# Optimization experiments

Hardware: AMD Instinct MI355X
Metric: run time of the kernel (lower is better)

## Reference

```python
import jax, jax.numpy as jnp
import numpy as np

N = 10000
E = 320000
NDIM_IN = 128
EDIM = 128
NDIM_OUT = 128
HID = 152  # size_embedding
NCLS = 15  # nbclasses


def _lin(k, out_f, in_f, scale=0.05):
    kw, kb = jax.random.split(k)
    W = jax.random.normal(kw, (out_f, in_f), dtype=jnp.float32) * scale
    b = jax.random.normal(kb, (out_f,), dtype=jnp.float32) * scale
    return W, b


def setup_inputs() -> dict:
    key = jax.random.key(0)
    ks = jax.random.split(key, 12)
    nfeats = jax.random.normal(ks[0], (N, 1, NDIM_IN), dtype=jnp.float32)
    efeats = jax.random.normal(ks[1], (E, 1, EDIM), dtype=jnp.float32)
    src = jax.random.randint(ks[2], (E,), 0, N)
    dst = jax.random.randint(ks[3], (E,), 0, N)
    # SAGE layer 1: msg (ndim_in+edim -> 152), apply (ndim_in+152 -> 152)
    Wm1, bm1 = _lin(ks[4], HID, NDIM_IN + EDIM)
    Wa1, ba1 = _lin(ks[5], HID, NDIM_IN + HID)
    # layer 2: msg (152+edim -> 152), apply (152+152 -> 152)
    Wm2, bm2 = _lin(ks[6], HID, HID + EDIM)
    Wa2, ba2 = _lin(ks[7], HID, HID + HID)
    # layer 3: msg (152+edim -> ndim_out), apply (152+ndim_out -> ndim_out)
    Wm3, bm3 = _lin(ks[8], NDIM_OUT, HID + EDIM)
    Wa3, ba3 = _lin(ks[9], NDIM_OUT, HID + NDIM_OUT)
    # edge predictor: Linear(2*ndim_out -> nbclasses)
    Wp, bp = _lin(ks[10], NCLS, 2 * NDIM_OUT)
    return {"nfeats": nfeats, "efeats": efeats, "src": src, "dst": dst,
            "Wm1": Wm1, "bm1": bm1, "Wa1": Wa1, "ba1": ba1,
            "Wm2": Wm2, "bm2": bm2, "Wa2": Wa2, "ba2": ba2,
            "Wm3": Wm3, "bm3": bm3, "Wa3": Wa3, "ba3": ba3,
            "Wp": Wp, "bp": bp}


def _sage_layer(h, e, src, dst, Wm, bm, Wa, ba):
    # h: [N,1,din]  e: [E,1,edim]
    msg = jnp.concatenate([h[src], e], axis=-1) @ Wm.T + bm  # [E,1,dout]
    agg = jax.ops.segment_sum(msg, dst, num_segments=N)       # [N,1,dout]
    deg = jax.ops.segment_sum(jnp.ones((E,), dtype=h.dtype), dst, num_segments=N)
    h_neigh = agg / jnp.maximum(deg, 1.0)[:, None, None]      # mean; 0 for isolated nodes
    return jax.nn.relu(jnp.concatenate([h, h_neigh], axis=-1) @ Wa.T + ba)


def reference(nfeats, efeats, src, dst,
              Wm1, bm1, Wa1, ba1, Wm2, bm2, Wa2, ba2,
              Wm3, bm3, Wa3, ba3, Wp, bp):
    h = _sage_layer(nfeats, efeats, src, dst, Wm1, bm1, Wa1, ba1)
    h = _sage_layer(h, efeats, src, dst, Wm2, bm2, Wa2, ba2)  # dropout is identity in eval
    h = _sage_layer(h, efeats, src, dst, Wm3, bm3, Wa3, ba3)
    h = h.sum(axis=1)  # [N, ndim_out]
    v = jnp.concatenate([h[src], h[dst]], axis=1)  # [E, 2*ndim_out]
    return v @ Wp.T + bp  # [E, nbclasses]
```

## Files before the change

### kernel.cpp

```cpp
#include <hip/hip_runtime.h>
#include <hip/hip_bf16.h>
#include <cstdint>


static inline int cdiv(int a, int b) { return (a + b - 1) / b; }

#define NN 10000
#define NE 320000
#define MTB 313

typedef __attribute__((ext_vector_type(8))) short bf16x8;
typedef __attribute__((ext_vector_type(4))) float f32x4;

__device__ __forceinline__ ushort f2bf(float x) {
  union { float f; unsigned u; } c; c.f = x;
  unsigned r = c.u + 0x7FFFu + ((c.u >> 16) & 1u);
  return (ushort)(r >> 16);
}
__device__ __forceinline__ float bf2f(unsigned h) {
  union { unsigned u; float f; } c; c.u = h << 16;
  return c.f;
}
__device__ __forceinline__ f32x4 mfma3(bf16x8 ah, bf16x8 al, bf16x8 bh, bf16x8 bl,
                                       f32x4 acc) {
  acc = __builtin_amdgcn_mfma_f32_16x16x32_bf16(ah, bh, acc, 0, 0, 0);
  acc = __builtin_amdgcn_mfma_f32_16x16x32_bf16(al, bh, acc, 0, 0, 0);
  acc = __builtin_amdgcn_mfma_f32_16x16x32_bf16(ah, bl, acc, 0, 0, 0);
  return acc;
}

__global__ __launch_bounds__(256) void k_hist(const int* __restrict__ dst,
                                              int* __restrict__ cnt) {
  int e = blockIdx.x * 256 + threadIdx.x;
  if (e < NE) atomicAdd(&cnt[dst[e]], 1);
}

__global__ __launch_bounds__(1024) void k_scan(const int* __restrict__ cnt,
                                               int* __restrict__ offs) {
  __shared__ int smem[1024];
  const int t = threadIdx.x;
  const int base = t * 10;
  int c[10];
  int s = 0;
#pragma unroll
  for (int i = 0; i < 10; ++i) {
    int idx = base + i;
    int v = (idx < NN) ? cnt[idx] : 0;
    s += v;
    c[i] = s;
  }
  smem[t] = s;
  __syncthreads();
  for (int ofs = 1; ofs < 1024; ofs <<= 1) {
    int add = (t >= ofs) ? smem[t - ofs] : 0;
    __syncthreads();
    smem[t] += add;
    __syncthreads();
  }
  int excl = smem[t] - s;
  if (t == 0) offs[0] = 0;
#pragma unroll
  for (int i = 0; i < 10; ++i) {
    int idx = base + i;
    if (idx < NN) offs[idx + 1] = excl + c[i];
  }
}

__global__ __launch_bounds__(256) void k_scatter(const int* __restrict__ src,
                                                 const int* __restrict__ dst,
                                                 const int* __restrict__ offs,
                                                 int* __restrict__ fill,
                                                 int* __restrict__ csr_edge,
                                                 int* __restrict__ csr_src) {
  int e = blockIdx.x * 256 + threadIdx.x;
  if (e < NE) {
    int d = dst[e];
    int pos = offs[d] + atomicAdd(&fill[d], 1);
    csr_edge[pos] = e;
    csr_src[pos] = src[e];
  }
}

struct WDesc {
  const float* W; ushort* hi; ushort* lo;
  int dout, KA, KApad, KB, Korig, NG16, KT, pred;
};
struct PrepArgs {
  WDesc d[7];
  const float* nf; ushort* nfh; ushort* nfl;
};

__global__ __launch_bounds__(256) void k_prep(PrepArgs P) {
  const int y = blockIdx.y;
  if (y == 7) {
    const int NTH = gridDim.x * 256;
    for (int i = blockIdx.x * 256 + threadIdx.x; i < NN * 32; i += NTH) {
      float4 v = ((const float4*)P.nf)[i];
      ushort h0 = f2bf(v.x), h1 = f2bf(v.y), h2 = f2bf(v.z), h3 = f2bf(v.w);
      uint2 uh, ul;
      uh.x = (unsigned)h0 | ((unsigned)h1 << 16);
      uh.y = (unsigned)h2 | ((unsigned)h3 << 16);
      ul.x = (unsigned)f2bf(v.x - bf2f(h0)) | ((unsigned)f2bf(v.y - bf2f(h1)) << 16);
      ul.y = (unsigned)f2bf(v.z - bf2f(h2)) | ((unsigned)f2bf(v.w - bf2f(h3)) << 16);
      ((uint2*)P.nfh)[i] = uh;
      ((uint2*)P.nfl)[i] = ul;
    }
    return;
  }
  const WDesc d = P.d[y];
  int tid = blockIdx.x * 256 + threadIdx.x;
  if (tid >= d.KT * d.NG16 * 64) return;
  int lane = tid & 63;
  int g = (tid >> 6) % d.NG16;
  int t = (tid >> 6) / d.NG16;
  int col = g * 16 + (lane & 15);
  int kbase = t * 32 + ((lane >> 4) * 8);
  size_t o = (size_t)tid * 8;
#pragma unroll
  for (int j = 0; j < 8; ++j) {
    int kk = kbase + j;
    float w = 0.f;
    if (!d.pred) {
      if (col < d.dout) {
        if (kk < d.KApad) { if (kk < d.KA) w = d.W[(size_t)col * d.Korig + kk]; }
        else { int kb = kk - d.KApad; if (kb < d.KB) w = d.W[(size_t)col * d.Korig + d.KA + kb]; }
      }
    } else {
      if (col < 15) w = d.W[(size_t)col * 256 + kk];
      else if (col < 30) w = d.W[(size_t)(col - 15) * 256 + 128 + kk];
    }
    ushort h = f2bf(w);
    d.hi[o + j] = h;
    d.lo[o + j] = f2bf(w - bf2f(h));
  }
}

__global__ __launch_bounds__(64) void k_eagg(const float* __restrict__ efeats,
                                             const int* __restrict__ csr_edge,
                                             const int* __restrict__ offs,
                                             ushort* __restrict__ ehi,
                                             ushort* __restrict__ elo,
                                             float* __restrict__ deg) {
  int d = blockIdx.x, lane = threadIdx.x;
  int s = offs[d], t = offs[d + 1];
  float2 a0 = make_float2(0.f, 0.f), a1 = a0, a2 = a0, a3 = a0;
  int j = s;
  for (; j + 7 < t; j += 8) {
    int e0 = csr_edge[j], e1 = csr_edge[j + 1], e2 = csr_edge[j + 2], e3 = csr_edge[j + 3];
    int e4 = csr_edge[j + 4], e5 = csr_edge[j + 5], e6 = csr_edge[j + 6], e7 = csr_edge[j + 7];
    float2 v0 = *(const float2*)(efeats + (size_t)e0 * 128 + lane * 2);
    float2 v1 = *(const float2*)(efeats + (size_t)e1 * 128 + lane * 2);
    float2 v2 = *(const float2*)(efeats + (size_t)e2 * 128 + lane * 2);
    float2 v3 = *(const float2*)(efeats + (size_t)e3 * 128 + lane * 2);
    float2 v4 = *(const float2*)(efeats + (size_t)e4 * 128 + lane * 2);
    float2 v5 = *(const float2*)(efeats + (size_t)e5 * 128 + lane * 2);
    float2 v6 = *(const float2*)(efeats + (size_t)e6 * 128 + lane * 2);
    float2 v7 = *(const float2*)(efeats + (size_t)e7 * 128 + lane * 2);
    a0.x += v0.x + v4.x; a0.y += v0.y + v4.y;
    a1.x += v1.x + v5.x; a1.y += v1.y + v5.y;
    a2.x += v2.x + v6.x; a2.y += v2.y + v6.y;
    a3.x += v3.x + v7.x; a3.y += v3.y + v7.y;
  }
  for (; j + 3 < t; j += 4) {
    int e0 = csr_edge[j], e1 = csr_edge[j + 1], e2 = csr_edge[j + 2], e3 = csr_edge[j + 3];
    float2 v0 = *(const float2*)(efeats + (size_t)e0 * 128 + lane * 2);
    float2 v1 = *(const float2*)(efeats + (size_t)e1 * 128 + lane * 2);
    float2 v2 = *(const float2*)(efeats + (size_t)e2 * 128 + lane * 2);
    float2 v3 = *(const float2*)(efeats + (size_t)e3 * 128 + lane * 2);
    a0.x += v0.x; a0.y += v0.y;
    a1.x += v1.x; a1.y += v1.y;
    a2.x += v2.x; a2.y += v2.y;
    a3.x += v3.x; a3.y += v3.y;
  }
  for (; j < t; ++j) {
    int e0 = csr_edge[j];
    float2 v0 = *(const float2*)(efeats + (size_t)e0 * 128 + lane * 2);
    a0.x += v0.x; a0.y += v0.y;
  }
  float sx = (a0.x + a1.x) + (a2.x + a3.x);
  float sy = (a0.y + a1.y) + (a2.y + a3.y);
  size_t o = (size_t)d * 128 + lane * 2;
  ushort hx = f2bf(sx), hy = f2bf(sy);
  ehi[o] = hx; ehi[o + 1] = hy;
  elo[o] = f2bf(sx - bf2f(hx)); elo[o + 1] = f2bf(sy - bf2f(hy));
  if (lane == 0) deg[d] = (float)(t - s);
}

__global__ __launch_bounds__(64) void k_projpe(
    const ushort* __restrict__ nfh, const ushort* __restrict__ nfl,
    const ushort* __restrict__ eah, const ushort* __restrict__ eal,
    const ushort* __restrict__ Wm1h, const ushort* __restrict__ Wm1l,
    const ushort* __restrict__ pW1h, const ushort* __restrict__ pW1l,
    const ushort* __restrict__ pW2h, const ushort* __restrict__ pW2l,
    const ushort* __restrict__ pW3h, const ushort* __restrict__ pW3l,
    const float* __restrict__ bm1, const float* __restrict__ bm2,
    const float* __restrict__ bm3, const float* __restrict__ deg,
    ushort* __restrict__ ph, float* __restrict__ pe1, float* __restrict__ pe2,
    float* __restrict__ pe3) {
  const int bx = blockIdx.x, lane = threadIdx.x;
  const ushort *Ah, *Al, *Wh, *Wl;
  const float* bm = nullptr;
  float* pe = nullptr;
  int NG16, ng0, WPAD = 160, dout;
  bool proj = false;
  if (bx < 5) {
    proj = true; Ah = nfh; Al = nfl; Wh = Wm1h; Wl = Wm1l;
    NG16 = 10; ng0 = bx * 2; dout = 152;
  } else if (bx < 10) {
    Ah = eah; Al = eal; Wh = pW1h; Wl = pW1l; bm = bm1; pe = pe1;
    NG16 = 10; ng0 = (bx - 5) * 2; dout = 152;
  } else if (bx < 15) {
    Ah = eah; Al = eal; Wh = pW2h; Wl = pW2l; bm = bm2; pe = pe2;
    NG16 = 10; ng0 = (bx - 10) * 2; dout = 152;
  } else {
    Ah = eah; Al = eal; Wh = pW3h; Wl = pW3l; bm = bm3; pe = pe3;
    NG16 = 8; ng0 = (bx - 15) * 2; WPAD = 128; dout = 128;
  }
  const int row0 = blockIdx.y * 32;
  const int rA = lane & 15, kl = (lane >> 4) * 8, colL = lane & 15;
  const int r0 = min(row0 + rA, NN - 1), r1 = min(row0 + 16 + rA, NN - 1);
  f32x4 a00 = {0.f, 0.f, 0.f, 0.f}, a01 = {0.f, 0.f, 0.f, 0.f};
  f32x4 a10 = {0.f, 0.f, 0.f, 0.f}, a11 = {0.f, 0.f, 0.f, 0.f};
#pragma unroll
  for (int kt = 0; kt < 4; ++kt) {
    size_t o0 = (size_t)r0 * 128 + kt * 32 + kl;
    size_t o1 = (size_t)r1 * 128 + kt * 32 + kl;
    bf16x8 a0h = *(const bf16x8*)(Ah + o0), a0l = *(const bf16x8*)(Al + o0);
    bf16x8 a1h = *(const bf16x8*)(Ah + o1), a1l = *(const bf16x8*)(Al + o1);
    size_t wb = ((size_t)(kt * NG16 + ng0) * 64 + lane) * 8;
    bf16x8 b0h = *(const bf16x8*)(Wh + wb), b0l = *(const bf16x8*)(Wl + wb);
    bf16x8 b1h = *(const bf16x8*)(Wh + wb + 512), b1l = *(const bf16x8*)(Wl + wb + 512);
    a00 = mfma3(a0h, a0l, b0h, b0l, a00);
    a01 = mfma3(a0h, a0l, b1h, b1l, a01);
    a10 = mfma3(a1h, a1l, b0h, b0l, a10);
    a11 = mfma3(a1h, a1l, b1h, b1l, a11);
  }
#pragma unroll
  for (int ms = 0; ms < 2; ++ms) {
    const f32x4 aN0 = ms ? a10 : a00;
    const f32x4 aN1 = ms ? a11 : a01;
#pragma unroll
    for (int reg = 0; reg < 4; ++reg) {
      int row = row0 + ms * 16 + (lane >> 4) * 4 + reg;
      if (row >= NN) continue;
#pragma unroll
      for (int ns = 0; ns < 2; ++ns) {
        int col = (ng0 + ns) * 16 + colL;
        float v = ns ? aN1[reg] : aN0[reg];
        if (proj) {
          ph[(size_t)row * 160 + col] = f2bf(col < 152 ? v : 0.f);
        } else {
          pe[(size_t)row * WPAD + col] = (col < dout) ? v + deg[row] * bm[col] : 0.f;
        }
      }
    }
  }
}

template <int WP>
__global__ __launch_bounds__(64) void k_gath(const ushort* __restrict__ ph,
                                             const float* __restrict__ pe,
                                             const float* __restrict__ deg,
                                             const int* __restrict__ cs,
                                             const int* __restrict__ offs,
                                             ushort* __restrict__ nmh,
                                             ushort* __restrict__ nml) {
  constexpr int PAIRS = WP / 2;
  constexpr int NV = (PAIRS + 63) / 64;
  const int d = blockIdx.x, lane = threadIdx.x;
  const int s = offs[d], t = offs[d + 1];
  float2 acc[NV][4];
#pragma unroll
  for (int v = 0; v < NV; ++v)
#pragma unroll
    for (int u = 0; u < 4; ++u) acc[v][u] = make_float2(0.f, 0.f);
  int j = s;
  for (; j + 3 < t; j += 4) {
    int s0 = cs[j], s1 = cs[j + 1], s2 = cs[j + 2], s3 = cs[j + 3];
#pragma unroll
    for (int v = 0; v < NV; ++v) {
      int p = lane + 64 * v;
      if (p < PAIRS) {
        unsigned x0 = *(const unsigned*)(ph + (size_t)s0 * WP + 2 * p);
        unsigned x1 = *(const unsigned*)(ph + (size_t)s1 * WP + 2 * p);
        unsigned x2 = *(const unsigned*)(ph + (size_t)s2 * WP + 2 * p);
        unsigned x3 = *(const unsigned*)(ph + (size_t)s3 * WP + 2 * p);
        acc[v][0].x += bf2f(x0 & 0xffffu); acc[v][0].y += bf2f(x0 >> 16);
        acc[v][1].x += bf2f(x1 & 0xffffu); acc[v][1].y += bf2f(x1 >> 16);
        acc[v][2].x += bf2f(x2 & 0xffffu); acc[v][2].y += bf2f(x2 >> 16);
        acc[v][3].x += bf2f(x3 & 0xffffu); acc[v][3].y += bf2f(x3 >> 16);
      }
    }
  }
  for (; j < t; ++j) {
    int s0 = cs[j];
#pragma unroll
    for (int v = 0; v < NV; ++v) {
      int p = lane + 64 * v;
      if (p < PAIRS) {
        unsigned x0 = *(const unsigned*)(ph + (size_t)s0 * WP + 2 * p);
        acc[v][0].x += bf2f(x0 & 0xffffu); acc[v][0].y += bf2f(x0 >> 16);
      }
    }
  }
  const float inv = 1.f / fmaxf(deg[d], 1.f);
#pragma unroll
  for (int v = 0; v < NV; ++v) {
    int p = lane + 64 * v;
    if (p < PAIRS) {
      float sx = (acc[v][0].x + acc[v][1].x) + (acc[v][2].x + acc[v][3].x);
      float sy = (acc[v][0].y + acc[v][1].y) + (acc[v][2].y + acc[v][3].y);
      float2 pv = *(const float2*)(pe + (size_t)d * WP + 2 * p);
      float nx = (sx + pv.x) * inv, ny = (sy + pv.y) * inv;
      size_t o = (size_t)d * WP + 2 * p;
      ushort hx = f2bf(nx), hy = f2bf(ny);
      *(unsigned*)(nmh + o) = (unsigned)hx | ((unsigned)hy << 16);
      *(unsigned*)(nml + o) =
          (unsigned)f2bf(nx - bf2f(hx)) | ((unsigned)f2bf(ny - bf2f(hy)) << 16);
    }
  }
}

template <int KTH, int KTNM, int NGA, int NGP, bool PRED>
__global__ __launch_bounds__(NGA * 32) void k_applyproj(
    const ushort* __restrict__ Ahi, const ushort* __restrict__ Alo,
    const ushort* __restrict__ nmh, const ushort* __restrict__ nml,
    const ushort* __restrict__ Wah, const ushort* __restrict__ Wal,
    const float* __restrict__ ba,
    ushort* __restrict__ Yhi, ushort* __restrict__ Ylo,
    const ushort* __restrict__ Wnh, const ushort* __restrict__ Wnl,
    ushort* __restrict__ phout, float* __restrict__ hsd,
    int dout_a, int dout_p) {
  constexpr int KTO = NGA / 2;
  constexpr int OSTR = KTO * 32;
  constexpr int SA = KTH * 32, SB = KTNM * 32;
  constexpr int OSTR2 = NGP * 16;
  __shared__ ushort lds[2 * KTO * 1024];
  const int tid = threadIdx.x;
  const int wid = tid >> 6, lane = tid & 63;
  const int rA = lane & 15, kl = (lane >> 4) * 8, colL = lane & 15;
  const int q = lane >> 4;
  const int row0 = blockIdx.x * 32;
  const int r0 = min(row0 + rA, NN - 1), r1 = min(row0 + 16 + rA, NN - 1);
  {
    const int ng0 = wid * 2;
    f32x4 a00 = {0.f, 0.f, 0.f, 0.f}, a01 = {0.f, 0.f, 0.f, 0.f};
    f32x4 a10 = {0.f, 0.f, 0.f, 0.f}, a11 = {0.f, 0.f, 0.f, 0.f};
#pragma unroll
    for (int kt = 0; kt < KTH + KTNM; ++kt) {
      bf16x8 a0h, a0l, a1h, a1l;
      if (kt < KTH) {
        size_t o0 = (size_t)r0 * SA + kt * 32 + kl;
        size_t o1 = (size_t)r1 * SA + kt * 32 + kl;
        a0h = *(const bf16x8*)(Ahi + o0); a0l = *(const bf16x8*)(Alo + o0);
        a1h = *(const bf16x8*)(Ahi + o1); a1l = *(const bf16x8*)(Alo + o1);
      } else {
        int kb = (kt - KTH) * 32 + kl;
        size_t o0 = (size_t)r0 * SB + kb, o1 = (size_t)r1 * SB + kb;
        a0h = *(const bf16x8*)(nmh + o0); a0l = *(const bf16x8*)(nml + o0);
        a1h = *(const bf16x8*)(nmh + o1); a1l = *(const bf16x8*)(nml + o1);
      }
      size_t wb = ((size_t)(kt * NGA + ng0) * 64 + lane) * 8;
      bf16x8 b0h = *(const bf16x8*)(Wah + wb), b0l = *(const bf16x8*)(Wal + wb);
      bf16x8 b1h = *(const bf16x8*)(Wah + wb + 512), b1l = *(const bf16x8*)(Wal + wb + 512);
      a00 = mfma3(a0h, a0l, b0h, b0l, a00);
      a01 = mfma3(a0h, a0l, b1h, b1l, a01);
      a10 = mfma3(a1h, a1l, b0h, b0l, a10);
      a11 = mfma3(a1h, a1l, b1h, b1l, a11);
    }
#pragma unroll
    for (int ms = 0; ms < 2; ++ms) {
      const f32x4 aN0 = ms ? a10 : a00;
      const f32x4 aN1 = ms ? a11 : a01;
#pragma unroll
      for (int reg = 0; reg < 4; ++reg) {
        int rloc = ms * 16 + (lane >> 4) * 4 + reg;
        int row = row0 + rloc;
#pragma unroll
        for (int ns = 0; ns < 2; ++ns) {
          int col = (ng0 + ns) * 16 + colL;
          float v = ns ? aN1[reg] : aN0[reg];
          float y = (col < dout_a) ? fmaxf(v + ba[col], 0.f) : 0.f;
          ushort h = f2bf(y), l = f2bf(y - bf2f(h));
          int idx = ((col >> 5) * 4 + ((col >> 3) & 3)) * 256 + rloc * 8 + (col & 7);
          lds[idx] = h;
          lds[idx + KTO * 1024] = l;
          if constexpr (!PRED) {
            if (row < NN) {
              Yhi[(size_t)row * OSTR + col] = h;
              Ylo[(size_t)row * OSTR + col] = l;
            }
          }
        }
      }
    }
  }
  __syncthreads();
  if (wid < NGP / 2) {
    const int ng0 = wid * 2;
    f32x4 a00 = {0.f, 0.f, 0.f, 0.f}, a01 = {0.f, 0.f, 0.f, 0.f};
    f32x4 a10 = {0.f, 0.f, 0.f, 0.f}, a11 = {0.f, 0.f, 0.f, 0.f};
#pragma unroll
    for (int kt = 0; kt < KTO; ++kt) {
      int b0 = (kt * 4 + q) * 256;
      int b1 = ((KTO + kt) * 4 + q) * 256;
      bf16x8 a0h = *(const bf16x8*)(lds + b0 + rA * 8);
      bf16x8 a1h = *(const bf16x8*)(lds + b0 + (rA + 16) * 8);
      bf16x8 a0l = *(const bf16x8*)(lds + b1 + rA * 8);
      bf16x8 a1l = *(const bf16x8*)(lds + b1 + (rA + 16) * 8);
      size_t wb = ((size_t)(kt * NGP + ng0) * 64 + lane) * 8;
      bf16x8 b0h = *(const bf16x8*)(Wnh + wb), b0l = *(const bf16x8*)(Wnl + wb);
      bf16x8 b1h = *(const bf16x8*)(Wnh + wb + 512), b1l = *(const bf16x8*)(Wnl + wb + 512);
      a00 = mfma3(a0h, a0l, b0h, b0l, a00);
      a01 = mfma3(a0h, a0l, b1h, b1l, a01);
      a10 = mfma3(a1h, a1l, b0h, b0l, a10);
      a11 = mfma3(a1h, a1l, b1h, b1l, a11);
    }
#pragma unroll
    for (int ms = 0; ms < 2; ++ms) {
      const f32x4 aN0 = ms ? a10 : a00;
      const f32x4 aN1 = ms ? a11 : a01;
#pragma unroll
      for (int reg = 0; reg < 4; ++reg) {
        int row = row0 + ms * 16 + (lane >> 4) * 4 + reg;
        if (row >= NN) continue;
#pragma unroll
        for (int ns = 0; ns < 2; ++ns) {
          int col = (ng0 + ns) * 16 + colL;
          float v = ns ? aN1[reg] : aN0[reg];
          if constexpr (PRED)
            hsd[(size_t)row * 32 + col] = v;
          else
            phout[(size_t)row * OSTR2 + col] = f2bf(col < dout_p ? v : 0.f);
        }
      }
    }
  }
}

__global__ __launch_bounds__(256) void k_edge_out(const int* __restrict__ src,
                                                  const int* __restrict__ dst,
                                                  const float* __restrict__ hsd,
                                                  const float* __restrict__ bp,
                                                  float* __restrict__ out) {
  int i = blockIdx.x * 256 + threadIdx.x;
  if (i >= NE * 15) return;
  int e = i / 15, c = i - e * 15;
  out[i] = hsd[(size_t)src[e] * 32 + c] + hsd[(size_t)dst[e] * 32 + 15 + c] + bp[c];
}

extern "C" void kernel_launch(void* const* d_in, const int* in_sizes, int n_in,
                              void* d_out, int out_size, void* d_ws, size_t ws_size,
                              hipStream_t stream) {
  const float* nfeats = (const float*)d_in[0];
  const float* efeats = (const float*)d_in[1];
  const int* src = (const int*)d_in[2];
  const int* dst = (const int*)d_in[3];
  const float* Wm1 = (const float*)d_in[4];
  const float* bm1 = (const float*)d_in[5];
  const float* Wa1 = (const float*)d_in[6];
  const float* ba1 = (const float*)d_in[7];
  const float* Wm2 = (const float*)d_in[8];
  const float* bm2 = (const float*)d_in[9];
  const float* Wa2 = (const float*)d_in[10];
  const float* ba2 = (const float*)d_in[11];
  const float* Wm3 = (const float*)d_in[12];
  const float* bm3 = (const float*)d_in[13];
  const float* Wa3 = (const float*)d_in[14];
  const float* ba3 = (const float*)d_in[15];
  const float* Wp = (const float*)d_in[16];
  const float* bp = (const float*)d_in[17];
  float* out = (float*)d_out;

  char* base = (char*)d_ws;
  size_t woff = 0;
  auto alloc = [&](size_t bytes) -> void* {
    void* p = base + woff;
    woff += (bytes + 255) & ~(size_t)255;
    return p;
  };
  int* cnt = (int*)alloc((size_t)2 * NN * 4);
  int* fill = cnt + NN;
  int* offs = (int*)alloc((size_t)(NN + 1) * 4);
  int* ce = (int*)alloc((size_t)NE * 4);
  int* cs = (int*)alloc((size_t)NE * 4);
  float* deg = (float*)alloc((size_t)NN * 4);
  auto aplane = [&](int w) { return (ushort*)alloc((size_t)NN * w * 2); };
  ushort* nfh = aplane(128); ushort* nfl = aplane(128);
  ushort* eah = aplane(128); ushort* eal = aplane(128);
  ushort* h1h = aplane(160); ushort* h1l = aplane(160);
  ushort* h2h = aplane(160); ushort* h2l = aplane(160);
  ushort* nmh = aplane(160); ushort* nml = aplane(160);
  ushort* ph = aplane(160);
  float* pe1 = (float*)alloc((size_t)NN * 160 * 4);
  float* pe2 = (float*)alloc((size_t)NN * 160 * 4);
  float* pe3 = (float*)alloc((size_t)NN * 128 * 4);
  float* hsd = (float*)alloc((size_t)NN * 32 * 4);
  auto wpk = [&](int kt, int ng) { return (ushort*)alloc((size_t)kt * ng * 512 * 2); };
  ushort* Wm1h = wpk(8, 10);  ushort* Wm1l = wpk(8, 10);
  ushort* Wa1h = wpk(9, 10);  ushort* Wa1l = wpk(9, 10);
  ushort* Wm2h = wpk(9, 10);  ushort* Wm2l = wpk(9, 10);
  ushort* Wa2h = wpk(10, 10); ushort* Wa2l = wpk(10, 10);
  ushort* Wm3h = wpk(9, 8);   ushort* Wm3l = wpk(9, 8);
  ushort* Wa3h = wpk(9, 8);   ushort* Wa3l = wpk(9, 8);
  ushort* Wpph = wpk(4, 2);   ushort* Wppl = wpk(4, 2);

  hipMemsetAsync(cnt, 0, (size_t)2 * NN * 4, stream);

  k_hist<<<cdiv(NE, 256), 256, 0, stream>>>(dst, cnt);
  k_scan<<<1, 1024, 0, stream>>>(cnt, offs);
  k_scatter<<<cdiv(NE, 256), 256, 0, stream>>>(src, dst, offs, fill, ce, cs);

  PrepArgs pa;
  pa.d[0] = {Wm1, Wm1h, Wm1l, 152, 128, 128, 128, 256, 10, 8, 0};
  pa.d[1] = {Wa1, Wa1h, Wa1l, 152, 128, 128, 152, 280, 10, 9, 0};
  pa.d[2] = {Wm2, Wm2h, Wm2l, 152, 152, 160, 128, 280, 10, 9, 0};
  pa.d[3] = {Wa2, Wa2h, Wa2l, 152, 152, 160, 152, 304, 10, 10, 0};
  pa.d[4] = {Wm3, Wm3h, Wm3l, 128, 152, 160, 128, 280, 8, 9, 0};
  pa.d[5] = {Wa3, Wa3h, Wa3l, 128, 152, 160, 128, 280, 8, 9, 0};
  pa.d[6] = {Wp, Wpph, Wppl, 32, 128, 128, 0, 256, 2, 4, 1};
  pa.nf = nfeats; pa.nfh = nfh; pa.nfl = nfl;
  k_prep<<<dim3(128, 8), 256, 0, stream>>>(pa);

  k_eagg<<<NN, 64, 0, stream>>>(efeats, ce, offs, eah, eal, deg);

  k_projpe<<<dim3(19, MTB), 64, 0, stream>>>(
      nfh, nfl, eah, eal, Wm1h, Wm1l,
      Wm1h + (size_t)4 * 10 * 512, Wm1l + (size_t)4 * 10 * 512,
      Wm2h + (size_t)5 * 10 * 512, Wm2l + (size_t)5 * 10 * 512,
      Wm3h + (size_t)5 * 8 * 512, Wm3l + (size_t)5 * 8 * 512,
      bm1, bm2, bm3, deg, ph, pe1, pe2, pe3);

  k_gath<160><<<NN, 64, 0, stream>>>(ph, pe1, deg, cs, offs, nmh, nml);
  k_applyproj<4, 5, 10, 10, false><<<MTB, 320, 0, stream>>>(
      nfh, nfl, nmh, nml, Wa1h, Wa1l, ba1, h1h, h1l, Wm2h, Wm2l, ph, nullptr, 152, 152);
  k_gath<160><<<NN, 64, 0, stream>>>(ph, pe2, deg, cs, offs, nmh, nml);
  k_applyproj<5, 5, 10, 8, false><<<MTB, 320, 0, stream>>>(
      h1h, h1l, nmh, nml, Wa2h, Wa2l, ba2, h2h, h2l, Wm3h, Wm3l, ph, nullptr, 152, 128);
  k_gath<128><<<NN, 64, 0, stream>>>(ph, pe3, deg, cs, offs, nmh, nml);
  k_applyproj<5, 4, 8, 2, true><<<MTB, 256, 0, stream>>>(
      h2h, h2l, nmh, nml, Wa3h, Wa3l, ba3, nullptr, nullptr, Wpph, Wppl, nullptr, hsd, 128, 32);

  k_edge_out<<<cdiv(NE * 15, 256), 256, 0, stream>>>(src, dst, hsd, bp, out);
}
```

Before: 240.2 us.

## Fuse neighbor gather-mean into apply/projection kernel via LDS staging

Measured after the change: 267.7 us. 11.4% more time.

```diff
diff --git a/kernel.cpp b/kernel.cpp
--- a/kernel.cpp
+++ b/kernel.cpp
@@ -27,6 +27,29 @@
   acc = __builtin_amdgcn_mfma_f32_16x16x32_bf16(al, bh, acc, 0, 0, 0);
   acc = __builtin_amdgcn_mfma_f32_16x16x32_bf16(ah, bl, acc, 0, 0, 0);
   return acc;
+}
+
+__device__ __forceinline__ void wpack4(ushort* lds, int base, int KT, int row,
+                                       int k0, float4 v) {
+  int idx0 = base + ((k0 >> 5) * 4 + ((k0 >> 3) & 3)) * 256 + row * 8 + (k0 & 7);
+  int idx1 = idx0 + KT * 1024;
+  ushort h0 = f2bf(v.x), h1 = f2bf(v.y), h2 = f2bf(v.z), h3 = f2bf(v.w);
+  uint2 uh, ul;
+  uh.x = (unsigned)h0 | ((unsigned)h1 << 16);
+  uh.y = (unsigned)h2 | ((unsigned)h3 << 16);
+  ushort l0 = f2bf(v.x - bf2f(h0)), l1 = f2bf(v.y - bf2f(h1));
+  ushort l2 = f2bf(v.z - bf2f(h2)), l3 = f2bf(v.w - bf2f(h3));
+  ul.x = (unsigned)l0 | ((unsigned)l1 << 16);
+  ul.y = (unsigned)l2 | ((unsigned)l3 << 16);
+  *reinterpret_cast<uint2*>(&lds[idx0]) = uh;
+  *reinterpret_cast<uint2*>(&lds[idx1]) = ul;
+}
+
+__device__ __forceinline__ bf16x8 rfrag(const ushort* lds, int base, int KT,
+                                        int plane, int kt, int lane, int mh) {
+  int idx = base + ((plane * KT + kt) * 4 + (lane >> 4)) * 256 +
+            ((lane & 15) + 16 * mh) * 8;
+  return *reinterpret_cast<const bf16x8*>(&lds[idx]);
 }
 
 __global__ __launch_bounds__(256) void k_hist(const int* __restrict__ dst,
@@ -136,53 +159,57 @@
 }
 
 __global__ __launch_bounds__(64) void k_eagg(const float* __restrict__ efeats,
-                                             const int* __restrict__ csr_edge,
+                                             const int* __restrict__ ce,
                                              const int* __restrict__ offs,
                                              ushort* __restrict__ ehi,
                                              ushort* __restrict__ elo,
                                              float* __restrict__ deg) {
-  int d = blockIdx.x, lane = threadIdx.x;
-  int s = offs[d], t = offs[d + 1];
-  float2 a0 = make_float2(0.f, 0.f), a1 = a0, a2 = a0, a3 = a0;
+  const int d = blockIdx.x, lane = threadIdx.x;
+  const int half = lane >> 5, cl = lane & 31;
+  const int s = offs[d], t = offs[d + 1];
+  float4 a0 = {0.f, 0.f, 0.f, 0.f}, a1 = a0, a2 = a0, a3 = a0;
   int j = s;
   for (; j + 7 < t; j += 8) {
-    int e0 = csr_edge[j], e1 = csr_edge[j + 1], e2 = csr_edge[j + 2], e3 = csr_edge[j + 3];
-    int e4 = csr_edge[j + 4], e5 = csr_edge[j + 5], e6 = csr_edge[j + 6], e7 = csr_edge[j + 7];
-    float2 v0 = *(const float2*)(efeats + (size_t)e0 * 128 + lane * 2);
-    float2 v1 = *(const float2*)(efeats + (size_t)e1 * 128 + lane * 2);
-    float2 v2 = *(const float2*)(efeats + (size_t)e2 * 128 + lane * 2);
-    float2 v3 = *(const float2*)(efeats + (size_t)e3 * 128 + lane * 2);
-    float2 v4 = *(const float2*)(efeats + (size_t)e4 * 128 + lane * 2);
-    float2 v5 = *(const float2*)(efeats + (size_t)e5 * 128 + lane * 2);
-    float2 v6 = *(const float2*)(efeats + (size_t)e6 * 128 + lane * 2);
-    float2 v7 = *(const float2*)(efeats + (size_t)e7 * 128 + lane * 2);
-    a0.x += v0.x + v4.x; a0.y += v0.y + v4.y;
-    a1.x += v1.x + v5.x; a1.y += v1.y + v5.y;
-    a2.x += v2.x + v6.x; a2.y += v2.y + v6.y;
-    a3.x += v3.x + v7.x; a3.y += v3.y + v7.y;
-  }
-  for (; j + 3 < t; j += 4) {
-    int e0 = csr_edge[j], e1 = csr_edge[j + 1], e2 = csr_edge[j + 2], e3 = csr_edge[j + 3];
-    float2 v0 = *(const float2*)(efeats + (size_t)e0 * 128 + lane * 2);
-    float2 v1 = *(const float2*)(efeats + (size_t)e1 * 128 + lane * 2);
-    float2 v2 = *(const float2*)(efeats + (size_t)e2 * 128 + lane * 2);
-    float2 v3 = *(const float2*)(efeats + (size_t)e3 * 128 + lane * 2);
-    a0.x += v0.x; a0.y += v0.y;
-    a1.x += v1.x; a1.y += v1.y;
-    a2.x += v2.x; a2.y += v2.y;
-    a3.x += v3.x; a3.y += v3.y;
-  }
-  for (; j < t; ++j) {
-    int e0 = csr_edge[j];
-    float2 v0 = *(const float2*)(efeats + (size_t)e0 * 128 + lane * 2);
-    a0.x += v0.x; a0.y += v0.y;
-  }
-  float sx = (a0.x + a1.x) + (a2.x + a3.x);
-  float sy = (a0.y + a1.y) + (a2.y + a3.y);
-  size_t o = (size_t)d * 128 + lane * 2;
-  ushort hx = f2bf(sx), hy = f2bf(sy);
-  ehi[o] = hx; ehi[o + 1] = hy;
-  elo[o] = f2bf(sx - bf2f(hx)); elo[o + 1] = f2bf(sy - bf2f(hy));
+    int e0 = ce[j + half], e1 = ce[j + 2 + half], e2 = ce[j + 4 + half], e3 = ce[j + 6 + half];
+    float4 v0 = *(const float4*)(efeats + (size_t)e0 * 128 + cl * 4);
+    float4 v1 = *(const float4*)(efeats + (size_t)e1 * 128 + cl * 4);
+    float4 v2 = *(const float4*)(efeats + (size_t)e2 * 128 + cl * 4);
+    float4 v3 = *(const float4*)(efeats + (size_t)e3 * 128 + cl * 4);
+    a0.x += v0.x; a0.y += v0.y; a0.z += v0.z; a0.w += v0.w;
+    a1.x += v1.x; a1.y += v1.y; a1.z += v1.z; a1.w += v1.w;
+    a2.x += v2.x; a2.y += v2.y; a2.z += v2.z; a2.w += v2.w;
+    a3.x += v3.x; a3.y += v3.y; a3.z += v3.z; a3.w += v3.w;
+  }
+  for (; j + 1 < t; j += 2) {
+    int e0 = ce[j + half];
+    float4 v0 = *(const float4*)(efeats + (size_t)e0 * 128 + cl * 4);
+    a0.x += v0.x; a0.y += v0.y; a0.z += v0.z; a0.w += v0.w;
+  }
+  if (j < t && half == 0) {
+    int e0 = ce[j];
+    float4 v0 = *(const float4*)(efeats + (size_t)e0 * 128 + cl * 4);
+    a0.x += v0.x; a0.y += v0.y; a0.z += v0.z; a0.w += v0.w;
+  }
+  float4 sm;
+  sm.x = (a0.x + a1.x) + (a2.x + a3.x);
+  sm.y = (a0.y + a1.y) + (a2.y + a3.y);
+  sm.z = (a0.z + a1.z) + (a2.z + a3.z);
+  sm.w = (a0.w + a1.w) + (a2.w + a3.w);
+  sm.x += __shfl_xor(sm.x, 32);
+  sm.y += __shfl_xor(sm.y, 32);
+  sm.z += __shfl_xor(sm.z, 32);
+  sm.w += __shfl_xor(sm.w, 32);
+  if (lane < 32) {
+    size_t o = (size_t)d * 128 + cl * 4;
+    ushort h0 = f2bf(sm.x), h1 = f2bf(sm.y), h2 = f2bf(sm.z), h3 = f2bf(sm.w);
+    uint2 uh, ul;
+    uh.x = (unsigned)h0 | ((unsigned)h1 << 16);
+    uh.y = (unsigned)h2 | ((unsigned)h3 << 16);
+    ul.x = (unsigned)f2bf(sm.x - bf2f(h0)) | ((unsigned)f2bf(sm.y - bf2f(h1)) << 16);
+    ul.y = (unsigned)f2bf(sm.z - bf2f(h2)) | ((unsigned)f2bf(sm.w - bf2f(h3)) << 16);
+    *(uint2*)(ehi + o) = uh;
+    *(uint2*)(elo + o) = ul;
+  }
   if (lane == 0) deg[d] = (float)(t - s);
 }
 
@@ -257,74 +284,12 @@
   }
 }
 
-template <int WP>
-__global__ __launch_bounds__(64) void k_gath(const ushort* __restrict__ ph,
-                                             const float* __restrict__ pe,
-                                             const float* __restrict__ deg,
-                                             const int* __restrict__ cs,
-                                             const int* __restrict__ offs,
-                                             ushort* __restrict__ nmh,
-                                             ushort* __restrict__ nml) {
-  constexpr int PAIRS = WP / 2;
-  constexpr int NV = (PAIRS + 63) / 64;
-  const int d = blockIdx.x, lane = threadIdx.x;
-  const int s = offs[d], t = offs[d + 1];
-  float2 acc[NV][4];
-#pragma unroll
-  for (int v = 0; v < NV; ++v)
-#pragma unroll
-    for (int u = 0; u < 4; ++u) acc[v][u] = make_float2(0.f, 0.f);
-  int j = s;
-  for (; j + 3 < t; j += 4) {
-    int s0 = cs[j], s1 = cs[j + 1], s2 = cs[j + 2], s3 = cs[j + 3];
-#pragma unroll
-    for (int v = 0; v < NV; ++v) {
-      int p = lane + 64 * v;
-      if (p < PAIRS) {
-        unsigned x0 = *(const unsigned*)(ph + (size_t)s0 * WP + 2 * p);
-        unsigned x1 = *(const unsigned*)(ph + (size_t)s1 * WP + 2 * p);
-        unsigned x2 = *(const unsigned*)(ph + (size_t)s2 * WP + 2 * p);
-        unsigned x3 = *(const unsigned*)(ph + (size_t)s3 * WP + 2 * p);
-        acc[v][0].x += bf2f(x0 & 0xffffu); acc[v][0].y += bf2f(x0 >> 16);
-        acc[v][1].x += bf2f(x1 & 0xffffu); acc[v][1].y += bf2f(x1 >> 16);
-        acc[v][2].x += bf2f(x2 & 0xffffu); acc[v][2].y += bf2f(x2 >> 16);
-        acc[v][3].x += bf2f(x3 & 0xffffu); acc[v][3].y += bf2f(x3 >> 16);
-      }
-    }
-  }
-  for (; j < t; ++j) {
-    int s0 = cs[j];
-#pragma unroll
-    for (int v = 0; v < NV; ++v) {
-      int p = lane + 64 * v;
-      if (p < PAIRS) {
-        unsigned x0 = *(const unsigned*)(ph + (size_t)s0 * WP + 2 * p);
-        acc[v][0].x += bf2f(x0 & 0xffffu); acc[v][0].y += bf2f(x0 >> 16);
-      }
-    }
-  }
-  const float inv = 1.f / fmaxf(deg[d], 1.f);
-#pragma unroll
-  for (int v = 0; v < NV; ++v) {
-    int p = lane + 64 * v;
-    if (p < PAIRS) {
-      float sx = (acc[v][0].x + acc[v][1].x) + (acc[v][2].x + acc[v][3].x);
-      float sy = (acc[v][0].y + acc[v][1].y) + (acc[v][2].y + acc[v][3].y);
-      float2 pv = *(const float2*)(pe + (size_t)d * WP + 2 * p);
-      float nx = (sx + pv.x) * inv, ny = (sy + pv.y) * inv;
-      size_t o = (size_t)d * WP + 2 * p;
-      ushort hx = f2bf(nx), hy = f2bf(ny);
-      *(unsigned*)(nmh + o) = (unsigned)hx | ((unsigned)hy << 16);
-      *(unsigned*)(nml + o) =
-          (unsigned)f2bf(nx - bf2f(hx)) | ((unsigned)f2bf(ny - bf2f(hy)) << 16);
-    }
-  }
-}
-
 template <int KTH, int KTNM, int NGA, int NGP, bool PRED>
-__global__ __launch_bounds__(NGA * 32) void k_applyproj(
+__global__ __launch_bounds__(512) void k_ga(
     const ushort* __restrict__ Ahi, const ushort* __restrict__ Alo,
-    const ushort* __restrict__ nmh, const ushort* __restrict__ nml,
+    const ushort* __restrict__ phin, const float* __restrict__ pe,
+    const float* __restrict__ deg, const int* __restrict__ cs,
+    const int* __restrict__ offs,
     const ushort* __restrict__ Wah, const ushort* __restrict__ Wal,
     const float* __restrict__ ba,
     ushort* __restrict__ Yhi, ushort* __restrict__ Ylo,
@@ -332,17 +297,59 @@
     ushort* __restrict__ phout, float* __restrict__ hsd,
     int dout_a, int dout_p) {
   constexpr int KTO = NGA / 2;
+  constexpr int WP = KTNM * 32;
+  constexpr int QUADS = WP / 4;
+  constexpr int SA = KTH * 32;
   constexpr int OSTR = KTO * 32;
-  constexpr int SA = KTH * 32, SB = KTNM * 32;
   constexpr int OSTR2 = NGP * 16;
-  __shared__ ushort lds[2 * KTO * 1024];
+  constexpr int BASE_OUT = 2 * KTNM * 1024;
+  __shared__ ushort lds[BASE_OUT + 2 * KTO * 1024];
   const int tid = threadIdx.x;
   const int wid = tid >> 6, lane = tid & 63;
+  const int row0 = blockIdx.x * 32;
+#pragma unroll
+  for (int i = 0; i < 4; ++i) {
+    const int r = wid * 4 + i;
+    const int gr = row0 + r;
+    float4 sm = {0.f, 0.f, 0.f, 0.f};
+    if (gr < NN && lane < QUADS) {
+      const int s = offs[gr], t = offs[gr + 1];
+      float4 a0 = {0.f, 0.f, 0.f, 0.f}, a1 = a0, a2 = a0, a3 = a0;
+      int j = s;
+      for (; j + 3 < t; j += 4) {
+        int s0 = cs[j], s1 = cs[j + 1], s2 = cs[j + 2], s3 = cs[j + 3];
+        uint2 u0 = *(const uint2*)(phin + (size_t)s0 * WP + 4 * lane);
+        uint2 u1 = *(const uint2*)(phin + (size_t)s1 * WP + 4 * lane);
+        uint2 u2 = *(const uint2*)(phin + (size_t)s2 * WP + 4 * lane);
+        uint2 u3 = *(const uint2*)(phin + (size_t)s3 * WP + 4 * lane);
+        a0.x += bf2f(u0.x & 0xffffu); a0.y += bf2f(u0.x >> 16);
+        a0.z += bf2f(u0.y & 0xffffu); a0.w += bf2f(u0.y >> 16);
+        a1.x += bf2f(u1.x & 0xffffu); a1.y += bf2f(u1.x >> 16);
+        a1.z += bf2f(u1.y & 0xffffu); a1.w += bf2f(u1.y >> 16);
+        a2.x += bf2f(u2.x & 0xffffu); a2.y += bf2f(u2.x >> 16);
+        a2.z += bf2f(u2.y & 0xffffu); a2.w += bf2f(u2.y >> 16);
+        a3.x += bf2f(u3.x & 0xffffu); a3.y += bf2f(u3.x >> 16);
+        a3.z += bf2f(u3.y & 0xffffu); a3.w += bf2f(u3.y >> 16);
+      }
+      for (; j < t; ++j) {
+        uint2 u0 = *(const uint2*)(phin + (size_t)cs[j] * WP + 4 * lane);
+        a0.x += bf2f(u0.x & 0xffffu); a0.y += bf2f(u0.x >> 16);
+        a0.z += bf2f(u0.y & 0xffffu); a0.w += bf2f(u0.y >> 16);
+      }
+      const float inv = 1.f / fmaxf(deg[gr], 1.f);
+      float4 pv = *(const float4*)(pe + (size_t)gr * WP + 4 * lane);
+      sm.x = ((a0.x + a1.x) + (a2.x + a3.x) + pv.x) * inv;
+      sm.y = ((a0.y + a1.y) + (a2.y + a3.y) + pv.y) * inv;
+      sm.z = ((a0.z + a1.z) + (a2.z + a3.z) + pv.z) * inv;
+      sm.w = ((a0.w + a1.w) + (a2.w + a3.w) + pv.w) * inv;
+    }
+    if (lane < QUADS) wpack4(lds, 0, KTNM, r, 4 * lane, sm);
+  }
+  __syncthreads();
   const int rA = lane & 15, kl = (lane >> 4) * 8, colL = lane & 15;
   const int q = lane >> 4;
-  const int row0 = blockIdx.x * 32;
   const int r0 = min(row0 + rA, NN - 1), r1 = min(row0 + 16 + rA, NN - 1);
-  {
+  if (wid < NGA / 2) {
     const int ng0 = wid * 2;
     f32x4 a00 = {0.f, 0.f, 0.f, 0.f}, a01 = {0.f, 0.f, 0.f, 0.f};
     f32x4 a10 = {0.f, 0.f, 0.f, 0.f}, a11 = {0.f, 0.f, 0.f, 0.f};
@@ -355,10 +362,11 @@
         a0h = *(const bf16x8*)(Ahi + o0); a0l = *(const bf16x8*)(Alo + o0);
         a1h = *(const bf16x8*)(Ahi + o1); a1l = *(const bf16x8*)(Alo + o1);
       } else {
-        int kb = (kt - KTH) * 32 + kl;
-        size_t o0 = (size_t)r0 * SB + kb, o1 = (size_t)r1 * SB + kb;
-        a0h = *(const bf16x8*)(nmh + o0); a0l = *(const bf16x8*)(nml + o0);
-        a1h = *(const bf16x8*)(nmh + o1); a1l = *(const bf16x8*)(nml + o1);
+        const int rkt = kt - KTH;
+        a0h = rfrag(lds, 0, KTNM, 0, rkt, lane, 0);
+        a0l = rfrag(lds, 0, KTNM, 1, rkt, lane, 0);
+        a1h = rfrag(lds, 0, KTNM, 0, rkt, lane, 1);
+        a1l = rfrag(lds, 0, KTNM, 1, rkt, lane, 1);
       }
       size_t wb = ((size_t)(kt * NGA + ng0) * 64 + lane) * 8;
       bf16x8 b0h = *(const bf16x8*)(Wah + wb), b0l = *(const bf16x8*)(Wal + wb);
@@ -382,7 +390,7 @@
           float v = ns ? aN1[reg] : aN0[reg];
           float y = (col < dout_a) ? fmaxf(v + ba[col], 0.f) : 0.f;
           ushort h = f2bf(y), l = f2bf(y - bf2f(h));
-          int idx = ((col >> 5) * 4 + ((col >> 3) & 3)) * 256 + rloc * 8 + (col & 7);
+          int idx = BASE_OUT + ((col >> 5) * 4 + ((col >> 3) & 3)) * 256 + rloc * 8 + (col & 7);
           lds[idx] = h;
           lds[idx + KTO * 1024] = l;
           if constexpr (!PRED) {
@@ -402,8 +410,8 @@
     f32x4 a10 = {0.f, 0.f, 0.f, 0.f}, a11 = {0.f, 0.f, 0.f, 0.f};
 #pragma unroll
     for (int kt = 0; kt < KTO; ++kt) {
-      int b0 = (kt * 4 + q) * 256;
-      int b1 = ((KTO + kt) * 4 + q) * 256;
+      int b0 = BASE_OUT + (kt * 4 + q) * 256;
+      int b1 = BASE_OUT + ((KTO + kt) * 4 + q) * 256;
       bf16x8 a0h = *(const bf16x8*)(lds + b0 + rA * 8);
       bf16x8 a1h = *(const bf16x8*)(lds + b0 + (rA + 16) * 8);
       bf16x8 a0l = *(const bf16x8*)(lds + b1 + rA * 8);
@@ -490,8 +498,7 @@
   ushort* eah = aplane(128); ushort* eal = aplane(128);
   ushort* h1h = aplane(160); ushort* h1l = aplane(160);
   ushort* h2h = aplane(160); ushort* h2l = aplane(160);
-  ushort* nmh = aplane(160); ushort* nml = aplane(160);
-  ushort* ph = aplane(160);
+  ushort* ph1 = aplane(160); ushort* ph2 = aplane(160);
   float* pe1 = (float*)alloc((size_t)NN * 160 * 4);
   float* pe2 = (float*)alloc((size_t)NN * 160 * 4);
   float* pe3 = (float*)alloc((size_t)NN * 128 * 4);
@@ -529,17 +536,17 @@
       Wm1h + (size_t)4 * 10 * 512, Wm1l + (size_t)4 * 10 * 512,
       Wm2h + (size_t)5 * 10 * 512, Wm2l + (size_t)5 * 10 * 512,
       Wm3h + (size_t)5 * 8 * 512, Wm3l + (size_t)5 * 8 * 512,
-      bm1, bm2, bm3, deg, ph, pe1, pe2, pe3);
-
-  k_gath<160><<<NN, 64, 0, stream>>>(ph, pe1, deg, cs, offs, nmh, nml);
-  k_applyproj<4, 5, 10, 10, false><<<MTB, 320, 0, stream>>>(
-      nfh, nfl, nmh, nml, Wa1h, Wa1l, ba1, h1h, h1l, Wm2h, Wm2l, ph, nullptr, 152, 152);
-  k_gath<160><<<NN, 64, 0, stream>>>(ph, pe2, deg, cs, offs, nmh, nml);
-  k_applyproj<5, 5, 10, 8, false><<<MTB, 320, 0, stream>>>(
-      h1h, h1l, nmh, nml, Wa2h, Wa2l, ba2, h2h, h2l, Wm3h, Wm3l, ph, nullptr, 152, 128);
-  k_gath<128><<<NN, 64, 0, stream>>>(ph, pe3, deg, cs, offs, nmh, nml);
-  k_applyproj<5, 4, 8, 2, true><<<MTB, 256, 0, stream>>>(
-      h2h, h2l, nmh, nml, Wa3h, Wa3l, ba3, nullptr, nullptr, Wpph, Wppl, nullptr, hsd, 128, 32);
+      bm1, bm2, bm3, deg, ph1, pe1, pe2, pe3);
+
+  k_ga<4, 5, 10, 10, false><<<MTB, 512, 0, stream>>>(
+      nfh, nfl, ph1, pe1, deg, cs, offs, Wa1h, Wa1l, ba1,
+      h1h, h1l, Wm2h, Wm2l, ph2, nullptr, 152, 152);
+  k_ga<5, 5, 10, 8, false><<<MTB, 512, 0, stream>>>(
+      h1h, h1l, ph2, pe2, deg, cs, offs, Wa2h, Wa2l, ba2,
+      h2h, h2l, Wm3h, Wm3l, ph1, nullptr, 152, 128);
+  k_ga<5, 4, 8, 2, true><<<MTB, 512, 0, stream>>>(
+      h2h, h2l, ph1, pe3, deg, cs, offs, Wa3h, Wa3l, ba3,
+      nullptr, nullptr, Wpph, Wppl, nullptr, hsd, 128, 32);
 
   k_edge_out<<<cdiv(NE * 15, 256), 256, 0, stream>>>(src, dst, hsd, bp, out);
 }
```
